# Performance work log

Measured on AMD Instinct MI355X. Metric: run time of the kernel, lower is better.

The kernel has to match this reference:

```python
import jax, jax.numpy as jnp
import numpy as np
from jax import lax

RADIUS = 4
SIGMA_1 = 5.0
SIGMA_2 = 1.0


def _gaussian_kernel_3d(radius, sigma):
    x = np.linspace(-radius, radius, 2 * radius + 1)
    xx, yy, zz = np.meshgrid(x, x, x)
    dist2 = xx ** 2 + yy ** 2 + zz ** 2
    k = np.exp(-dist2 / (2.0 * sigma ** 2)).astype(np.float32)
    return jnp.asarray(k)[None, None]  # [O=1, I=1, D, H, W]


def _conv3d_same(x, kernel, radius):
    # x: [B,1,D,H,W], kernel: [1,1,kd,kh,kw]
    pad = [(radius, radius)] * 3
    return lax.conv_general_dilated(
        x, kernel, window_strides=(1, 1, 1), padding=pad,
        dimension_numbers=('NCDHW', 'OIDHW', 'NCDHW'))


def setup_inputs() -> dict:
    key = jax.random.key(0)
    k1, k2 = jax.random.split(key)
    labels = jax.random.uniform(k1, (4, 1, 160, 160, 160), dtype=jnp.float32)
    inputs = jax.random.uniform(k2, (4, 1, 160, 160, 160), dtype=jnp.float32)
    return {"labels": labels, "inputs": inputs}


def reference(labels, inputs):
    kernel = _gaussian_kernel_3d(RADIUS, SIGMA_1)
    num_classes = 2
    p0 = labels[:, 0:1]  # [B,1,D,H,W]
    loss = jnp.float32(0.0)
    for k in range(num_classes):
        class_probs = p0 if k == 0 else 1.0 - p0
        class_mean = (jnp.mean(inputs * class_probs, axis=(2, 3, 4), keepdims=True)
                      / (jnp.mean(class_probs, axis=(2, 3, 4), keepdims=True) + 1e-5))
        diff = jnp.sum((inputs - class_mean) ** 2, axis=1, keepdims=True)  # [B,1,D,H,W]
        weights = jnp.exp(-(diff ** 2) / (SIGMA_2 ** 2))
        numerator = jnp.sum(class_probs * _conv3d_same(class_probs * weights, kernel, RADIUS))
        denominator = jnp.sum(class_probs * _conv3d_same(weights, kernel, RADIUS))
        # L1Loss(scalar, 0) == abs(scalar)
        loss = loss + jnp.abs(numerator / (denominator + 1e-6))
    return jnp.float32(num_classes) - loss
```

## Files before the change

kernel.cpp:

```cpp
#include <hip/hip_runtime.h>
#include <hip/hip_fp16.h>
#include <math.h>

#define NX   160
#define N2   25600
#define N3   4096000
#define NB   4

#define ZPB  4
#define NBLK_XY 4000
#define BLKS_PER_B 1000
#define NBLK_Z 800

#define SB_W 36
#define SB_PLANE (40 * SB_W)

__device__ __constant__ float G1[9] = {
    0.72614903f, 0.83527021f, 0.92311635f, 0.98019867f, 1.0f,
    0.98019867f, 0.92311635f, 0.83527021f, 0.72614903f};

#define ES_FULL 7.92946852f
__device__ __constant__ float ES_M[4] = {3.46473426f, 2.48453559f, 1.56141924f,
                                         0.72614903f};
__device__ inline float edge_sum(int i) {
    float s = ES_FULL;
    if (i < 4) s -= ES_M[i];
    if (i > NX - 5) s -= ES_M[NX - 1 - i];
    return s;
}

__device__ inline float4 f4_zero() { return make_float4(0.f, 0.f, 0.f, 0.f); }
__device__ inline float4 f4_axpy(float a, float4 b, float4 c) {
    return make_float4(c.x + a * b.x, c.y + a * b.y, c.z + a * b.z, c.w + a * b.w);
}

__device__ inline float4 load_t4(const __half* p) {
    uint2 u = *(const uint2*)p;
    __half2 a = *(const __half2*)&u.x;
    __half2 b = *(const __half2*)&u.y;
    float2 fa = __half22float2(a);
    float2 fb = __half22float2(b);
    return make_float4(fa.x, fa.y, fb.x, fb.y);
}

template <int NV>
__device__ inline void block_reduce_store(double* vals, double* dst) {
    __shared__ double red[4][NV];
    int lane = threadIdx.x & 63;
    int wave = threadIdx.x >> 6;
#pragma unroll
    for (int v = 0; v < NV; ++v) {
        double x = vals[v];
#pragma unroll
        for (int off = 32; off > 0; off >>= 1) x += __shfl_down(x, off, 64);
        if (lane == 0) red[wave][v] = x;
    }
    __syncthreads();
    if (threadIdx.x < NV) {
        int v = threadIdx.x;
        dst[v] = red[0][v] + red[1][v] + red[2][v] + red[3][v];
    }
}

__global__ __launch_bounds__(256) void conv_xy_kernel(
    const float* __restrict__ labels, const float* __restrict__ inputs,
    __half* __restrict__ t, double* __restrict__ pS) {
    __shared__ float sB[ZPB * SB_PLANE];

    int bid = blockIdx.x;
    int tileX = bid % 5;
    int tileY = (bid / 5) % 5;
    int zq = (bid / 25) % 40;
    int b = bid / BLKS_PER_B;
    int zbase = zq * ZPB;
    int x0 = tileX * 32, y0 = tileY * 32;
    int tid = threadIdx.x;
    int baseOff = b * N3 + zbase * N2;

    for (int i = tid; i < ZPB * 320; i += 256) {
        int j = i / 320;
        int rem = i - 320 * j;
        int r = rem >> 3, x4 = rem & 7;
        int gy = y0 + r - 4;
        int gxf = x0 + 4 * x4 - 4;
        float w[12];
        if (gy >= 0 && gy < NX) {
            const float* row = &labels[baseOff + j * N2 + gy * NX];
#pragma unroll
            for (int c = 0; c < 3; ++c) {
                int gx = gxf + 4 * c;
                float4 v = (gx >= 0 && gx <= NX - 4) ? *(const float4*)&row[gx]
                                                     : f4_zero();
                w[4 * c] = v.x; w[4 * c + 1] = v.y;
                w[4 * c + 2] = v.z; w[4 * c + 3] = v.w;
            }
        } else {
#pragma unroll
            for (int c = 0; c < 12; ++c) w[c] = 0.f;
        }
        float4 o = f4_zero();
#pragma unroll
        for (int d = 0; d < 9; ++d) {
            float g = G1[d];
            o.x += g * w[d];
            o.y += g * w[d + 1];
            o.z += g * w[d + 2];
            o.w += g * w[d + 3];
        }
        *(float4*)&sB[j * SB_PLANE + r * SB_W + 4 * x4] = o;
    }
    __syncthreads();

    int oy = tid >> 3, x4 = tid & 7;
    double sp = 0.0, sip = 0.0, si = 0.0;
#pragma unroll
    for (int j = 0; j < ZPB; ++j) {
        float4 acc = f4_zero();
#pragma unroll
        for (int d = 0; d < 9; ++d) {
            float4 v = *(const float4*)&sB[j * SB_PLANE + (oy + d) * SB_W + 4 * x4];
            acc = f4_axpy(G1[d], v, acc);
        }
        int gi = baseOff + j * N2 + (y0 + oy) * NX + (x0 + 4 * x4);
        __half2 ha = __floats2half2_rn(acc.x, acc.y);
        __half2 hb = __floats2half2_rn(acc.z, acc.w);
        uint2 u;
        u.x = *(unsigned int*)&ha;
        u.y = *(unsigned int*)&hb;
        *(uint2*)&t[gi] = u;

        float4 p = *(const float4*)&labels[gi];
        float4 in = *(const float4*)&inputs[gi];
        sp += (double)(p.x + p.y + p.z + p.w);
        sip += (double)(in.x * p.x + in.y * p.y + in.z * p.z + in.w * p.w);
        si += (double)(in.x + in.y + in.z + in.w);
    }
    double vals[3] = {sp, sip, si};
    block_reduce_store<3>(vals, pS + 3 * bid);
}

__global__ __launch_bounds__(256) void reduce_S_kernel(
    const double* __restrict__ pS, double* __restrict__ S) {
    int b = blockIdx.x;
    double v0 = 0, v1 = 0, v2 = 0;
    for (int i = threadIdx.x; i < BLKS_PER_B; i += 256) {
        const double* p = pS + 3 * (b * BLKS_PER_B + i);
        v0 += p[0]; v1 += p[1]; v2 += p[2];
    }
    double vals[3] = {v0, v1, v2};
    block_reduce_store<3>(vals, S + 3 * b);
}

__global__ __launch_bounds__(256) void conv_z_kernel(
    const __half* __restrict__ t, const float* __restrict__ labels,
    const float* __restrict__ inputs, const double* __restrict__ S,
    double* __restrict__ pZ) {
    int tid = threadIdx.x;
    int tidg = blockIdx.x * 256 + tid;
    int x4 = tidg % 40;
    int r = tidg / 40;
    int y = r % NX;
    r /= NX;
    int zc = r % 8;
    int b = r / 8;

    double sp = S[3 * b + 0], sip = S[3 * b + 1], si = S[3 * b + 2];
    const double Nv = (double)N3;
    float m0 = (float)((sip / Nv) / (sp / Nv + 1e-5));
    float m1 = (float)(((si - sip) / Nv) / ((Nv - sp) / Nv + 1e-5));

    int x = x4 * 4;
    float ey = edge_sum(y);
    float cx[4] = {edge_sum(x) * ey, edge_sum(x + 1) * ey,
                   edge_sum(x + 2) * ey, edge_sum(x + 3) * ey};

    int z0 = zc * 20;
    int base = b * N3 + y * NX + x;

    float4 win[9];
#pragma unroll
    for (int d = 0; d < 9; ++d) {
        int z = z0 - 4 + d;
        win[d] = (z >= 0 && z < NX) ? load_t4(&t[base + z * N2]) : f4_zero();
    }

    float n0 = 0.f, d0 = 0.f, n1 = 0.f, d1 = 0.f;
    for (int zb5 = 0; zb5 < 5; ++zb5) {
        int z = z0 + 4 * zb5;
        float4 tn[4], pv[4], iv[4];
#pragma unroll
        for (int j = 0; j < 4; ++j) {
            int zl = z + j + 5;
            tn[j] = (zl < NX) ? load_t4(&t[base + zl * N2]) : f4_zero();
            int gi = base + (z + j) * N2;
            pv[j] = *(const float4*)&labels[gi];
            iv[j] = *(const float4*)&inputs[gi];
        }
#pragma unroll
        for (int j = 0; j < 4; ++j) {
            float4 c4 = f4_zero();
#pragma unroll
            for (int d = 0; d < 9; ++d) c4 = f4_axpy(G1[d], win[d], c4);
            float ez = edge_sum(z + j);
            float pc[4] = {pv[j].x, pv[j].y, pv[j].z, pv[j].w};
            float ic[4] = {iv[j].x, iv[j].y, iv[j].z, iv[j].w};
            float cc[4] = {c4.x, c4.y, c4.z, c4.w};
#pragma unroll
            for (int l = 0; l < 4; ++l) {
                float c1 = cx[l] * ez - cc[l];
                float df0 = ic[l] - m0; df0 *= df0;
                float w0 = __expf(-df0 * df0);
                float df1 = ic[l] - m1; df1 *= df1;
                float w1 = __expf(-df1 * df1);
                n0 += cc[l] * pc[l] * w0;
                d0 += cc[l] * w0;
                n1 += c1 * (1.f - pc[l]) * w1;
                d1 += c1 * w1;
            }
#pragma unroll
            for (int d = 0; d < 8; ++d) win[d] = win[d + 1];
            win[8] = tn[j];
        }
    }
    double vals[4] = {(double)n0, (double)d0, (double)n1, (double)d1};
    block_reduce_store<4>(vals, pZ + 4 * blockIdx.x);
}

__global__ __launch_bounds__(256) void finalize_kernel(
    const double* __restrict__ pZ, float* __restrict__ out) {
    double a0 = 0, a1 = 0, a2 = 0, a3 = 0;
    for (int i = threadIdx.x; i < NBLK_Z; i += 256) {
        const double* p = &pZ[4 * i];
        a0 += p[0]; a1 += p[1]; a2 += p[2]; a3 += p[3];
    }
    __shared__ double red[4][4];
    int lane = threadIdx.x & 63;
    int wave = threadIdx.x >> 6;
    double vals[4] = {a0, a1, a2, a3};
#pragma unroll
    for (int v = 0; v < 4; ++v) {
        double x = vals[v];
#pragma unroll
        for (int off = 32; off > 0; off >>= 1) x += __shfl_down(x, off, 64);
        if (lane == 0) red[wave][v] = x;
    }
    __syncthreads();
    if (threadIdx.x == 0) {
        double acc[4];
#pragma unroll
        for (int v = 0; v < 4; ++v)
            acc[v] = red[0][v] + red[1][v] + red[2][v] + red[3][v];
        double r0 = fabs(acc[0] / (acc[1] + 1e-6));
        double r1 = fabs(acc[2] / (acc[3] + 1e-6));
        out[0] = (float)(2.0 - r0 - r1);
    }
}

extern "C" void kernel_launch(void* const* d_in, const int* in_sizes, int n_in,
                              void* d_out, int out_size, void* d_ws, size_t ws_size,
                              hipStream_t stream) {
    const float* labels = (const float*)d_in[0];
    const float* inputs = (const float*)d_in[1];
    float* out = (float*)d_out;

    double* pS = (double*)d_ws;
    double* S  = (double*)((char*)d_ws + 96000);
    double* pZ = (double*)((char*)d_ws + 96128);
    __half* t  = (__half*)((char*)d_ws + 524288);

    hipLaunchKernelGGL(conv_xy_kernel, dim3(NBLK_XY), dim3(256), 0, stream,
                       labels, inputs, t, pS);
    hipLaunchKernelGGL(reduce_S_kernel, dim3(NB), dim3(256), 0, stream, pS, S);
    hipLaunchKernelGGL(conv_z_kernel, dim3(NBLK_Z), dim3(256), 0, stream,
                       t, labels, inputs, S, pZ);
    hipLaunchKernelGGL(finalize_kernel, dim3(1), dim3(256), 0, stream, pZ, out);
}
```

Before: 198.7 us.

## Replace shared-memory XY tiling with register sliding window along Y

The XY convolution no longer stages x-convolved rows in shared memory. Each thread now owns a 4-wide column strip over a chunk of 20 Y rows and keeps a 9-row register window of x-convolved values that slides down the strip, so each halo row is read and x-convolved once per chunk instead of once per tile. The partial sums are accumulated in float rather than double, and the block count and workspace offsets shrink to match. In exchange each thread holds more registers, there are only 800 blocks, and the float accumulation loses some precision.

```diff
diff --git a/kernel.cpp b/kernel.cpp
--- a/kernel.cpp
+++ b/kernel.cpp
@@ -7,13 +7,10 @@
 #define N3   4096000
 #define NB   4
 
-#define ZPB  4
-#define NBLK_XY 4000
-#define BLKS_PER_B 1000
+#define YCH  20
+#define NBLK_XY 800
+#define BLKS_PER_B_XY 200
 #define NBLK_Z 800
-
-#define SB_W 36
-#define SB_PLANE (40 * SB_W)
 
 __device__ __constant__ float G1[9] = {
     0.72614903f, 0.83527021f, 0.92311635f, 0.98019867f, 1.0f,
@@ -43,6 +40,20 @@
     return make_float4(fa.x, fa.y, fb.x, fb.y);
 }
 
+__device__ inline float4 xconv9(float4 a, float4 b, float4 c) {
+    float w[12] = {a.x, a.y, a.z, a.w, b.x, b.y, b.z, b.w, c.x, c.y, c.z, c.w};
+    float4 o = f4_zero();
+#pragma unroll
+    for (int d = 0; d < 9; ++d) {
+        float g = G1[d];
+        o.x += g * w[d];
+        o.y += g * w[d + 1];
+        o.z += g * w[d + 2];
+        o.w += g * w[d + 3];
+    }
+    return o;
+}
+
 template <int NV>
 __device__ inline void block_reduce_store(double* vals, double* dst) {
     __shared__ double red[4][NV];
@@ -65,86 +76,87 @@
 __global__ __launch_bounds__(256) void conv_xy_kernel(
     const float* __restrict__ labels, const float* __restrict__ inputs,
     __half* __restrict__ t, double* __restrict__ pS) {
-    __shared__ float sB[ZPB * SB_PLANE];
-
-    int bid = blockIdx.x;
-    int tileX = bid % 5;
-    int tileY = (bid / 5) % 5;
-    int zq = (bid / 25) % 40;
-    int b = bid / BLKS_PER_B;
-    int zbase = zq * ZPB;
-    int x0 = tileX * 32, y0 = tileY * 32;
     int tid = threadIdx.x;
-    int baseOff = b * N3 + zbase * N2;
-
-    for (int i = tid; i < ZPB * 320; i += 256) {
-        int j = i / 320;
-        int rem = i - 320 * j;
-        int r = rem >> 3, x4 = rem & 7;
-        int gy = y0 + r - 4;
-        int gxf = x0 + 4 * x4 - 4;
-        float w[12];
+    int tidg = blockIdx.x * 256 + tid;
+    int x4 = tidg % 40;
+    int r = tidg / 40;
+    int z = r % NX;
+    r /= NX;
+    int yc = r % 8;
+    int b = r / 8;
+    int y0 = yc * YCH;
+
+    bool v0 = (x4 > 0);
+    bool v2 = (x4 < 39);
+    int colbase = b * N3 + z * N2 + 4 * x4;
+    const float* rowp = labels + colbase;
+    const float* inp = inputs + colbase;
+
+    float4 win[9];
+#pragma unroll
+    for (int d = 0; d < 9; ++d) {
+        int gy = y0 - 4 + d;
         if (gy >= 0 && gy < NX) {
-            const float* row = &labels[baseOff + j * N2 + gy * NX];
-#pragma unroll
-            for (int c = 0; c < 3; ++c) {
-                int gx = gxf + 4 * c;
-                float4 v = (gx >= 0 && gx <= NX - 4) ? *(const float4*)&row[gx]
-                                                     : f4_zero();
-                w[4 * c] = v.x; w[4 * c + 1] = v.y;
-                w[4 * c + 2] = v.z; w[4 * c + 3] = v.w;
-            }
+            const float* p = rowp + gy * NX;
+            float4 a = v0 ? *(const float4*)(p - 4) : f4_zero();
+            float4 bb = *(const float4*)p;
+            float4 c = v2 ? *(const float4*)(p + 4) : f4_zero();
+            win[d] = xconv9(a, bb, c);
         } else {
-#pragma unroll
-            for (int c = 0; c < 12; ++c) w[c] = 0.f;
-        }
-        float4 o = f4_zero();
-#pragma unroll
-        for (int d = 0; d < 9; ++d) {
-            float g = G1[d];
-            o.x += g * w[d];
-            o.y += g * w[d + 1];
-            o.z += g * w[d + 2];
-            o.w += g * w[d + 3];
-        }
-        *(float4*)&sB[j * SB_PLANE + r * SB_W + 4 * x4] = o;
-    }
-    __syncthreads();
-
-    int oy = tid >> 3, x4 = tid & 7;
-    double sp = 0.0, sip = 0.0, si = 0.0;
-#pragma unroll
-    for (int j = 0; j < ZPB; ++j) {
-        float4 acc = f4_zero();
-#pragma unroll
-        for (int d = 0; d < 9; ++d) {
-            float4 v = *(const float4*)&sB[j * SB_PLANE + (oy + d) * SB_W + 4 * x4];
-            acc = f4_axpy(G1[d], v, acc);
-        }
-        int gi = baseOff + j * N2 + (y0 + oy) * NX + (x0 + 4 * x4);
-        __half2 ha = __floats2half2_rn(acc.x, acc.y);
-        __half2 hb = __floats2half2_rn(acc.z, acc.w);
-        uint2 u;
-        u.x = *(unsigned int*)&ha;
-        u.y = *(unsigned int*)&hb;
-        *(uint2*)&t[gi] = u;
-
-        float4 p = *(const float4*)&labels[gi];
-        float4 in = *(const float4*)&inputs[gi];
-        sp += (double)(p.x + p.y + p.z + p.w);
-        sip += (double)(in.x * p.x + in.y * p.y + in.z * p.z + in.w * p.w);
-        si += (double)(in.x + in.y + in.z + in.w);
-    }
-    double vals[3] = {sp, sip, si};
-    block_reduce_store<3>(vals, pS + 3 * bid);
+            win[d] = f4_zero();
+        }
+    }
+
+    float sp = 0.f, sip = 0.f, si = 0.f;
+#pragma unroll
+    for (int g = 0; g < YCH / 4; ++g) {
+        int yb = y0 + 4 * g;
+        float4 ra[4], rb[4], rc[4], pv[4], iv[4];
+#pragma unroll
+        for (int j = 0; j < 4; ++j) {
+            int rr = yb + 5 + j;
+            bool vr = (rr < NX);
+            const float* p = rowp + rr * NX;
+            ra[j] = (vr && v0) ? *(const float4*)(p - 4) : f4_zero();
+            rb[j] = vr ? *(const float4*)p : f4_zero();
+            rc[j] = (vr && v2) ? *(const float4*)(p + 4) : f4_zero();
+            pv[j] = *(const float4*)(rowp + (yb + j) * NX);
+            iv[j] = *(const float4*)(inp + (yb + j) * NX);
+        }
+#pragma unroll
+        for (int j = 0; j < 4; ++j) {
+            float4 o = f4_zero();
+#pragma unroll
+            for (int d = 0; d < 9; ++d) o = f4_axpy(G1[d], win[d], o);
+            int gi = colbase + (yb + j) * NX;
+            __half2 ha = __floats2half2_rn(o.x, o.y);
+            __half2 hb = __floats2half2_rn(o.z, o.w);
+            uint2 u;
+            u.x = *(unsigned int*)&ha;
+            u.y = *(unsigned int*)&hb;
+            *(uint2*)&t[gi] = u;
+
+            sp += pv[j].x + pv[j].y + pv[j].z + pv[j].w;
+            sip += iv[j].x * pv[j].x + iv[j].y * pv[j].y +
+                   iv[j].z * pv[j].z + iv[j].w * pv[j].w;
+            si += iv[j].x + iv[j].y + iv[j].z + iv[j].w;
+
+            float4 nx = xconv9(ra[j], rb[j], rc[j]);
+#pragma unroll
+            for (int d = 0; d < 8; ++d) win[d] = win[d + 1];
+            win[8] = nx;
+        }
+    }
+    double vals[3] = {(double)sp, (double)sip, (double)si};
+    block_reduce_store<3>(vals, pS + 3 * blockIdx.x);
 }
 
 __global__ __launch_bounds__(256) void reduce_S_kernel(
     const double* __restrict__ pS, double* __restrict__ S) {
     int b = blockIdx.x;
     double v0 = 0, v1 = 0, v2 = 0;
-    for (int i = threadIdx.x; i < BLKS_PER_B; i += 256) {
-        const double* p = pS + 3 * (b * BLKS_PER_B + i);
+    for (int i = threadIdx.x; i < BLKS_PER_B_XY; i += 256) {
+        const double* p = pS + 3 * (b * BLKS_PER_B_XY + i);
         v0 += p[0]; v1 += p[1]; v2 += p[2];
     }
     double vals[3] = {v0, v1, v2};
@@ -264,8 +276,8 @@
     float* out = (float*)d_out;
 
     double* pS = (double*)d_ws;
-    double* S  = (double*)((char*)d_ws + 96000);
-    double* pZ = (double*)((char*)d_ws + 96128);
+    double* S  = (double*)((char*)d_ws + 19200);
+    double* pZ = (double*)((char*)d_ws + 19456);
     __half* t  = (__half*)((char*)d_ws + 524288);
 
     hipLaunchKernelGGL(conv_xy_kernel, dim3(NBLK_XY), dim3(256), 0, stream,
```

Result: slower. 221.8 us (+11.6%).
